# Kernel tuning notes

Measured on AMD Instinct MI355X. Metric: run time of the kernel, lower is better.

## Reference

```python
import jax, jax.numpy as jnp
import numpy as np

NACTIVE = 2048
FEATSIZE = 4096

def setup_inputs() -> dict:
    key = jax.random.key(0)
    feat = jax.random.normal(key, (16384, FEATSIZE), dtype=jnp.float32)
    return {"feat": feat}

def reference(feat) -> jnp.ndarray:
    # Training-mode MaxoutDynamic: zero the (featsize - nactive) smallest
    # features per row, scale survivors by featsize/nactive.
    B, F = feat.shape
    scale = jnp.asarray(F / NACTIVE, dtype=feat.dtype)  # 1/(1-proportion)
    n_drop = F - NACTIVE
    # ascending argsort; first n_drop columns are the smallest per row
    drop_idx = jnp.argsort(feat, axis=1)[:, :n_drop]          # [B, n_drop]
    rows = jnp.arange(B)[:, None]                             # [B, 1]
    out = feat.at[rows, drop_idx].set(0.0) * scale
    return out
```

## Files before the change

### kernel.cpp

```cpp
#include <hip/hip_runtime.h>


#define FEAT   4096
#define NDROP  2048
#define TPB    256
#define NBIN   1024
#define CAP    512

__global__ __launch_bounds__(TPB)
void MaxoutDynamic_55181739819231_kernel(const float* __restrict__ in,
                                         float* __restrict__ out) {
    const int row = blockIdx.x;
    const int t   = threadIdx.x;
    const float4* inrow  = (const float4*)(in  + (size_t)row * FEAT);
    float4*       outrow = (float4*)      (out + (size_t)row * FEAT);

    __shared__ unsigned int hist[NBIN];
    __shared__ float        list[CAP];
    __shared__ unsigned int s_cnt;
    __shared__ unsigned int s_bin;
    __shared__ unsigned int s_rank;
    __shared__ float        s_tau;

    float xs[16];
#pragma unroll
    for (int j = 0; j < 4; ++j) {
        float4 l = inrow[t + j * TPB];
        xs[4 * j + 0] = l.x;
        xs[4 * j + 1] = l.y;
        xs[4 * j + 2] = l.z;
        xs[4 * j + 3] = l.w;
    }

#pragma unroll
    for (int j = 0; j < 4; ++j) hist[t + j * TPB] = 0u;
    if (t == 0) { s_cnt = 0u; s_tau = 0.0f; }
    __syncthreads();

#pragma unroll
    for (int i = 0; i < 16; ++i) {
        int b = (int)((xs[i] + 4.0f) * 128.0f);
        b = b < 0 ? 0 : (b > (NBIN - 1) ? (NBIN - 1) : b);
        atomicAdd(&hist[b], 1u);
    }
    __syncthreads();

    if (t < 64) {
        unsigned int c[16];
        unsigned int sum = 0u;
#pragma unroll
        for (int i = 0; i < 16; ++i) { c[i] = hist[t * 16 + i]; sum += c[i]; }
        unsigned int incl = sum;
#pragma unroll
        for (int d = 1; d < 64; d <<= 1) {
            unsigned int y = __shfl_up(incl, d, 64);
            if (t >= d) incl += y;
        }
        unsigned int excl = incl - sum;
        if ((unsigned)NDROP >= excl && (unsigned)NDROP < excl + sum) {
            unsigned int rr = (unsigned)NDROP - excl;
            int bsel = 0, found = 0;
#pragma unroll
            for (int i = 0; i < 16; ++i) {
                if (!found) {
                    if (rr < c[i]) { bsel = i; found = 1; }
                    else rr -= c[i];
                }
            }
            s_bin  = (unsigned)(t * 16 + bsel);
            s_rank = rr;
        }
    }
    __syncthreads();

    const unsigned int selbin = s_bin;
#pragma unroll
    for (int i = 0; i < 16; ++i) {
        int b = (int)((xs[i] + 4.0f) * 128.0f);
        b = b < 0 ? 0 : (b > (NBIN - 1) ? (NBIN - 1) : b);
        if ((unsigned)b == selbin) {
            unsigned int idx = atomicAdd(&s_cnt, 1u);
            if (idx < CAP) list[idx] = xs[i];
        }
    }
    __syncthreads();

    if (t < 64) {
        int n = (int)s_cnt; if (n > CAP) n = CAP;
        const unsigned int rr = s_rank;
        for (int c0 = t; c0 < n; c0 += 64) {
            float vc = list[c0];
            unsigned int r = 0u, m = 0u;
            for (int j = 0; j < n; ++j) {
                float vj = list[j];
                r += (vj < vc) ? 1u : 0u;
                m += (vj == vc) ? 1u : 0u;
            }
            if (r <= rr && rr < r + m) s_tau = vc;
        }
    }
    __syncthreads();
    const float tau = s_tau;

#pragma unroll
    for (int j = 0; j < 4; ++j) {
        float4 o;
        o.x = (xs[4 * j + 0] >= tau) ? 2.0f * xs[4 * j + 0] : 0.0f;
        o.y = (xs[4 * j + 1] >= tau) ? 2.0f * xs[4 * j + 1] : 0.0f;
        o.z = (xs[4 * j + 2] >= tau) ? 2.0f * xs[4 * j + 2] : 0.0f;
        o.w = (xs[4 * j + 3] >= tau) ? 2.0f * xs[4 * j + 3] : 0.0f;
        outrow[t + j * TPB] = o;
    }
}

extern "C" void kernel_launch(void* const* d_in, const int* in_sizes, int n_in,
                              void* d_out, int out_size, void* d_ws, size_t ws_size,
                              hipStream_t stream) {
    const float* feat = (const float*)d_in[0];
    float* out = (float*)d_out;
    const int rows = in_sizes[0] / FEAT;
    MaxoutDynamic_55181739819231_kernel<<<rows, TPB, 0, stream>>>(feat, out);
}
```

Before: 423.7 us.

## Use ballot-counted narrow window histogram around median with full-range fallback

Before building any histogram, the kernel counts with wave ballots how many values fall below a narrow window around zero and how many fall inside it. If the median lies in that window, a fine 256-bin histogram is built over the window only, so fewer atomics are issued and the selected bin holds fewer candidates for the quadratic rank search. Otherwise it falls back to a coarser 256-bin histogram over [-4,4). Output stores become nontemporal. The window is tuned to the expected median of standard-normal rows, and the fallback path's coarser bins could overflow the candidate list.

```diff
diff --git a/kernel.cpp b/kernel.cpp
--- a/kernel.cpp
+++ b/kernel.cpp
@@ -4,112 +4,199 @@
 #define FEAT   4096
 #define NDROP  2048
 #define TPB    256
-#define NBIN   1024
+#define NBIN   256
 #define CAP    512
+#define WL     (-0.16f)
+#define WU     (0.16f)
+#define WSCALE (800.0f)
+
+typedef float v4f __attribute__((ext_vector_type(4)));
 
 __global__ __launch_bounds__(TPB)
 void MaxoutDynamic_55181739819231_kernel(const float* __restrict__ in,
                                          float* __restrict__ out) {
     const int row = blockIdx.x;
     const int t   = threadIdx.x;
-    const float4* inrow  = (const float4*)(in  + (size_t)row * FEAT);
-    float4*       outrow = (float4*)      (out + (size_t)row * FEAT);
+    const v4f* inrow  = (const v4f*)(in  + (size_t)row * FEAT);
+    v4f*       outrow = (v4f*)      (out + (size_t)row * FEAT);
 
     __shared__ unsigned int hist[NBIN];
     __shared__ float        list[CAP];
-    __shared__ unsigned int s_cnt;
-    __shared__ unsigned int s_bin;
-    __shared__ unsigned int s_rank;
+    __shared__ unsigned int wbelow[4], wwin[4];
+    __shared__ unsigned int s_cnt, s_bin, s_rank;
     __shared__ float        s_tau;
 
     float xs[16];
 #pragma unroll
     for (int j = 0; j < 4; ++j) {
-        float4 l = inrow[t + j * TPB];
+        v4f l = inrow[t + j * TPB];
         xs[4 * j + 0] = l.x;
         xs[4 * j + 1] = l.y;
         xs[4 * j + 2] = l.z;
         xs[4 * j + 3] = l.w;
     }
 
-#pragma unroll
-    for (int j = 0; j < 4; ++j) hist[t + j * TPB] = 0u;
+    unsigned int cb = 0u, cw = 0u;
+#pragma unroll
+    for (int i = 0; i < 16; ++i) {
+        cb += (unsigned int)__popcll(__ballot(xs[i] < WL));
+        cw += (unsigned int)__popcll(__ballot(xs[i] >= WL && xs[i] < WU));
+    }
+    if ((t & 63) == 0) { wbelow[t >> 6] = cb; wwin[t >> 6] = cw; }
+
+    hist[t] = 0u;
     if (t == 0) { s_cnt = 0u; s_tau = 0.0f; }
     __syncthreads();
 
-#pragma unroll
-    for (int i = 0; i < 16; ++i) {
-        int b = (int)((xs[i] + 4.0f) * 128.0f);
-        b = b < 0 ? 0 : (b > (NBIN - 1) ? (NBIN - 1) : b);
-        atomicAdd(&hist[b], 1u);
-    }
-    __syncthreads();
-
-    if (t < 64) {
-        unsigned int c[16];
-        unsigned int sum = 0u;
-#pragma unroll
-        for (int i = 0; i < 16; ++i) { c[i] = hist[t * 16 + i]; sum += c[i]; }
-        unsigned int incl = sum;
-#pragma unroll
-        for (int d = 1; d < 64; d <<= 1) {
-            unsigned int y = __shfl_up(incl, d, 64);
-            if (t >= d) incl += y;
-        }
-        unsigned int excl = incl - sum;
-        if ((unsigned)NDROP >= excl && (unsigned)NDROP < excl + sum) {
-            unsigned int rr = (unsigned)NDROP - excl;
-            int bsel = 0, found = 0;
-#pragma unroll
-            for (int i = 0; i < 16; ++i) {
-                if (!found) {
-                    if (rr < c[i]) { bsel = i; found = 1; }
-                    else rr -= c[i];
+    const unsigned int below = wbelow[0] + wbelow[1] + wbelow[2] + wbelow[3];
+    const unsigned int nwin  = wwin[0]  + wwin[1]  + wwin[2]  + wwin[3];
+
+    if (below <= (unsigned)NDROP && (unsigned)NDROP < below + nwin) {
+#pragma unroll
+        for (int i = 0; i < 16; ++i) {
+            if (xs[i] >= WL && xs[i] < WU) {
+                int b = (int)((xs[i] - WL) * WSCALE);
+                b = b < 0 ? 0 : (b > (NBIN - 1) ? (NBIN - 1) : b);
+                atomicAdd(&hist[b], 1u);
+            }
+        }
+        __syncthreads();
+
+        if (t < 64) {
+            unsigned int c0 = hist[4 * t + 0];
+            unsigned int c1 = hist[4 * t + 1];
+            unsigned int c2 = hist[4 * t + 2];
+            unsigned int c3 = hist[4 * t + 3];
+            unsigned int sum = c0 + c1 + c2 + c3;
+            unsigned int incl = sum;
+#pragma unroll
+            for (int d = 1; d < 64; d <<= 1) {
+                unsigned int y = __shfl_up(incl, d, 64);
+                if (t >= d) incl += y;
+            }
+            unsigned int excl = incl - sum;
+            unsigned int rr = (unsigned)NDROP - below;
+            if (rr >= excl && rr < excl + sum) {
+                rr -= excl;
+                unsigned int d;
+                if (rr < c0) { d = 0u; }
+                else { rr -= c0;
+                    if (rr < c1) { d = 1u; }
+                    else { rr -= c1;
+                        if (rr < c2) { d = 2u; }
+                        else { rr -= c2; d = 3u; } } }
+                s_bin  = 4u * (unsigned int)t + d;
+                s_rank = rr;
+            }
+        }
+        __syncthreads();
+
+        const unsigned int selbin = s_bin;
+#pragma unroll
+        for (int i = 0; i < 16; ++i) {
+            if (xs[i] >= WL && xs[i] < WU) {
+                int b = (int)((xs[i] - WL) * WSCALE);
+                b = b < 0 ? 0 : (b > (NBIN - 1) ? (NBIN - 1) : b);
+                if ((unsigned)b == selbin) {
+                    unsigned int idx = atomicAdd(&s_cnt, 1u);
+                    if (idx < CAP) list[idx] = xs[i];
                 }
             }
-            s_bin  = (unsigned)(t * 16 + bsel);
-            s_rank = rr;
-        }
-    }
-    __syncthreads();
-
-    const unsigned int selbin = s_bin;
-#pragma unroll
-    for (int i = 0; i < 16; ++i) {
-        int b = (int)((xs[i] + 4.0f) * 128.0f);
-        b = b < 0 ? 0 : (b > (NBIN - 1) ? (NBIN - 1) : b);
-        if ((unsigned)b == selbin) {
-            unsigned int idx = atomicAdd(&s_cnt, 1u);
-            if (idx < CAP) list[idx] = xs[i];
-        }
-    }
-    __syncthreads();
-
-    if (t < 64) {
-        int n = (int)s_cnt; if (n > CAP) n = CAP;
-        const unsigned int rr = s_rank;
-        for (int c0 = t; c0 < n; c0 += 64) {
-            float vc = list[c0];
-            unsigned int r = 0u, m = 0u;
-            for (int j = 0; j < n; ++j) {
-                float vj = list[j];
-                r += (vj < vc) ? 1u : 0u;
-                m += (vj == vc) ? 1u : 0u;
-            }
-            if (r <= rr && rr < r + m) s_tau = vc;
-        }
-    }
-    __syncthreads();
+        }
+        __syncthreads();
+
+        if (t < 64) {
+            int n = (int)s_cnt; if (n > CAP) n = CAP;
+            const unsigned int rr = s_rank;
+            for (int c = t; c < n; c += 64) {
+                float vc = list[c];
+                unsigned int r = 0u, m = 0u;
+                for (int j = 0; j < n; ++j) {
+                    float vj = list[j];
+                    r += (vj < vc) ? 1u : 0u;
+                    m += (vj == vc) ? 1u : 0u;
+                }
+                if (r <= rr && rr < r + m) s_tau = vc;
+            }
+        }
+        __syncthreads();
+    } else {
+        hist[t] = 0u;
+        if (t == 0) s_cnt = 0u;
+        __syncthreads();
+#pragma unroll
+        for (int i = 0; i < 16; ++i) {
+            int b = (int)((xs[i] + 4.0f) * 32.0f);
+            b = b < 0 ? 0 : (b > (NBIN - 1) ? (NBIN - 1) : b);
+            atomicAdd(&hist[b], 1u);
+        }
+        __syncthreads();
+        if (t < 64) {
+            unsigned int c0 = hist[4 * t + 0];
+            unsigned int c1 = hist[4 * t + 1];
+            unsigned int c2 = hist[4 * t + 2];
+            unsigned int c3 = hist[4 * t + 3];
+            unsigned int sum = c0 + c1 + c2 + c3;
+            unsigned int incl = sum;
+#pragma unroll
+            for (int d = 1; d < 64; d <<= 1) {
+                unsigned int y = __shfl_up(incl, d, 64);
+                if (t >= d) incl += y;
+            }
+            unsigned int excl = incl - sum;
+            unsigned int rr = (unsigned)NDROP;
+            if (rr >= excl && rr < excl + sum) {
+                rr -= excl;
+                unsigned int d;
+                if (rr < c0) { d = 0u; }
+                else { rr -= c0;
+                    if (rr < c1) { d = 1u; }
+                    else { rr -= c1;
+                        if (rr < c2) { d = 2u; }
+                        else { rr -= c2; d = 3u; } } }
+                s_bin  = 4u * (unsigned int)t + d;
+                s_rank = rr;
+            }
+        }
+        __syncthreads();
+        const unsigned int selbin = s_bin;
+#pragma unroll
+        for (int i = 0; i < 16; ++i) {
+            int b = (int)((xs[i] + 4.0f) * 32.0f);
+            b = b < 0 ? 0 : (b > (NBIN - 1) ? (NBIN - 1) : b);
+            if ((unsigned)b == selbin) {
+                unsigned int idx = atomicAdd(&s_cnt, 1u);
+                if (idx < CAP) list[idx] = xs[i];
+            }
+        }
+        __syncthreads();
+        if (t < 64) {
+            int n = (int)s_cnt; if (n > CAP) n = CAP;
+            const unsigned int rr = s_rank;
+            for (int c = t; c < n; c += 64) {
+                float vc = list[c];
+                unsigned int r = 0u, m = 0u;
+                for (int j = 0; j < n; ++j) {
+                    float vj = list[j];
+                    r += (vj < vc) ? 1u : 0u;
+                    m += (vj == vc) ? 1u : 0u;
+                }
+                if (r <= rr && rr < r + m) s_tau = vc;
+            }
+        }
+        __syncthreads();
+    }
+
     const float tau = s_tau;
 
 #pragma unroll
     for (int j = 0; j < 4; ++j) {
-        float4 o;
+        v4f o;
         o.x = (xs[4 * j + 0] >= tau) ? 2.0f * xs[4 * j + 0] : 0.0f;
         o.y = (xs[4 * j + 1] >= tau) ? 2.0f * xs[4 * j + 1] : 0.0f;
         o.z = (xs[4 * j + 2] >= tau) ? 2.0f * xs[4 * j + 2] : 0.0f;
         o.w = (xs[4 * j + 3] >= tau) ? 2.0f * xs[4 * j + 3] : 0.0f;
-        outrow[t + j * TPB] = o;
+        __builtin_nontemporal_store(o, &outrow[t + j * TPB]);
     }
 }
 
```

Measured after the change: 438.4 us. +3.5%, slower.
